# Kernel optimization log

Measured on AMD Instinct MI355X. Metric: run time of the kernel, lower is better.

Reference implementation:

```python
import jax, jax.numpy as jnp
import numpy as np

B, C, H, W, K = 64, 64, 32, 32, 512  # batch, embedding_dim, latent HxW, num_embeddings
COMMITMENT_COST = 0.25


def setup_inputs() -> dict:
    key = jax.random.key(0)
    k1, k2 = jax.random.split(key)
    inputs = jax.random.normal(k1, (B, C, H, W), dtype=jnp.float32)
    # nn.Embedding weight initialized uniform(-1/K, 1/K)
    weight = jax.random.uniform(k2, (K, C), minval=-1.0 / K, maxval=1.0 / K, dtype=jnp.float32)
    return {"inputs": inputs, "weight": weight}


def reference(inputs, weight):
    # NCHW -> NHWC
    x = jnp.transpose(inputs, (0, 2, 3, 1))  # [B,H,W,C]
    b, h, w, c = x.shape
    flat = x.reshape(-1, c)  # [N, C], N = B*H*W

    distances = (jnp.sum(flat * flat, axis=1, keepdims=True)
                 + jnp.sum(weight * weight, axis=1)[None, :]
                 - 2.0 * flat @ weight.T)

    idx = jnp.argmin(distances, axis=1)  # [N]
    encodings = jax.nn.one_hot(idx, weight.shape[0], dtype=flat.dtype)  # [N, K]

    # gather codebook vectors (same math as encodings @ weight)
    quantized = weight[idx].reshape(x.shape)  # [B,H,W,C]

    e_latent = jnp.mean((jax.lax.stop_gradient(quantized) - x) ** 2, axis=(1, 2, 3))
    q_latent = jnp.mean((quantized - jax.lax.stop_gradient(x)) ** 2, axis=(1, 2, 3))
    loss = q_latent + COMMITMENT_COST * e_latent  # [B]

    # straight-through estimator
    quantized_st = x + jax.lax.stop_gradient(quantized - x)

    avg_probs = jnp.mean(encodings, axis=0)  # [K]
    perplexity = jnp.exp(-jnp.sum(avg_probs * jnp.log(avg_probs + 1e-10)))

    q_out = jnp.transpose(quantized_st, (0, 3, 1, 2))  # back to NCHW
    enc_idx = idx.reshape(b, -1)  # [B, H*W]
    return (q_out, loss, perplexity, encodings, enc_idx, distances)
```

## Files before the change

kernel.cpp:

```cpp
#include <hip/hip_runtime.h>
#include <stdint.h>
#include <math.h>

#pragma clang fp contract(off)

#define B_   64
#define C_   64
#define HW_  1024
#define K_   512
#define N_   65536

#define OUT_Q    0ull
#define OUT_LOSS 4194304ull
#define OUT_PERP 4194368ull
#define OUT_ENC  4194369ull
#define OUT_IDX  37748801ull
#define OUT_DIST 37814337ull

#define WS_WT     0ull
#define WS_WNORM  131072ull
#define WS_HIST   133120ull
#define WS_SUMSQ  135168ull
#define WS_ZERO_BYTES (512*4 + 64*4)

__global__ __launch_bounds__(256) void vq_prep(const float* __restrict__ w,
                                               float* __restrict__ wt,
                                               float* __restrict__ wnorm) {
  const int t = threadIdx.x;
  const int g = blockIdx.x * 256 + t;
  const int c = g >> 9;
  const int k = g & 511;
  wt[g] = w[k * 64 + c];

  if (blockIdx.x < 16) {
    const int row = g >> 3;
    const int j = g & 7;
    float s = 0.f;
    for (int i = 0; i < 8; ++i) {
      float v = w[row * 64 + 8 * i + j];
      float sq = v * v;
      s = s + sq;
    }
    float o1 = __shfl_xor(s, 1); s = s + o1;
    float o2 = __shfl_xor(s, 2); s = s + o2;
    float o4 = __shfl_xor(s, 4); s = s + o4;
    if (j == 0) wnorm[row] = s;
  }
}

__global__ __launch_bounds__(256, 3) void vq_main(const float* __restrict__ x,
                                                  const float* __restrict__ wt,
                                                  const float* __restrict__ wnorm,
                                                  float* __restrict__ out,
                                                  int* __restrict__ hist,
                                                  float* __restrict__ sumsq) {
  __shared__ float x_s[64 * 32];
  __shared__ float w_s[16 * 512];
  __shared__ float wn_s[512];
  __shared__ float an_s[32];
  __shared__ int   kmin_s[32];
  __shared__ float red_s[4];

  const int t   = threadIdx.x;
  const int blk = blockIdx.x;
  const int n0  = blk * 32;
  const int b   = n0 >> 10;
  const int hw0 = n0 & 1023;
  const int wid = t >> 6;
  const int l   = t & 63;

  {
    const float* xb = x + (size_t)b * 65536 + hw0;
    const int c0 = t >> 3;
    const int m4 = (t & 7) * 4;
    for (int i = 0; i < 2; ++i) {
      int c = i * 32 + c0;
      float4 v = *(const float4*)(xb + (size_t)c * 1024 + m4);
      *(float4*)(&x_s[c * 32 + m4]) = v;
    }
  }
  wn_s[t] = wnorm[t];
  wn_s[t + 256] = wnorm[t + 256];
  __syncthreads();

  {
    const int r = t >> 3, j = t & 7;
    float s = 0.f;
    for (int i = 0; i < 8; ++i) {
      float v = x_s[(8 * i + j) * 32 + r];
      float sq = v * v;
      s = s + sq;
    }
    float o1 = __shfl_xor(s, 1); s = s + o1;
    float o2 = __shfl_xor(s, 2); s = s + o2;
    float o4 = __shfl_xor(s, 4); s = s + o4;
    if (j == 0) an_s[r] = s;
  }

  float wn[8];
  for (int j = 0; j < 8; ++j) wn[j] = wn_s[l + 64 * j];

  float acc[8][8];
  for (int i = 0; i < 8; ++i)
    for (int j = 0; j < 8; ++j) acc[i][j] = 0.f;

#pragma unroll 1
  for (int cc = 0; cc < 4; ++cc) {
    __syncthreads();
    for (int i = 0; i < 8; ++i) {
      int f4 = i * 256 + t;
      *(float4*)(&w_s[f4 * 4]) = *(const float4*)(wt + (size_t)cc * 8192 + f4 * 4);
    }
    __syncthreads();
#pragma unroll
    for (int cl = 0; cl < 16; ++cl) {
      const int c = cc * 16 + cl;
      float xv[8];
      *(float4*)(xv)     = *(const float4*)(&x_s[c * 32 + 8 * wid]);
      *(float4*)(xv + 4) = *(const float4*)(&x_s[c * 32 + 8 * wid + 4]);
      float wv[8];
      for (int j = 0; j < 8; ++j) wv[j] = w_s[cl * 512 + l + 64 * j];
      for (int i = 0; i < 8; ++i)
        for (int j = 0; j < 8; ++j)
          acc[i][j] = __builtin_fmaf(xv[i], wv[j], acc[i][j]);
    }
  }

  float* const dist_o = out + OUT_DIST;
  float* const enc_o  = out + OUT_ENC;
  const int m_base = 8 * wid;
  for (int i = 0; i < 8; ++i) {
    const int m = m_base + i;
    const size_t n = (size_t)(n0 + m);
    const float an = an_s[m];
    float D[8];
    for (int j = 0; j < 8; ++j) {
      float tt = an + wn[j];
      D[j] = __builtin_fmaf(-2.f, acc[i][j], tt);
    }
    float vb = D[0]; int kb = l;
    for (int j = 1; j < 8; ++j) {
      if (D[j] < vb) { vb = D[j]; kb = l + 64 * j; }
    }
    for (int d = 1; d < 64; d <<= 1) {
      float v2 = __shfl_xor(vb, d);
      int   k2 = __shfl_xor(kb, d);
      if (v2 < vb || (v2 == vb && k2 < kb)) { vb = v2; kb = k2; }
    }
    const size_t rb = n * 512 + l;
    for (int j = 0; j < 8; ++j) dist_o[rb + 64 * j] = D[j];
    for (int j = 0; j < 8; ++j) enc_o[rb + 64 * j] = (l + 64 * j == kb) ? 1.f : 0.f;
    if (l == i) {
      out[OUT_IDX + n] = (float)kb;
      atomicAdd(&hist[kb], 1);
      kmin_s[m] = kb;
    }
  }
  __syncthreads();

  float lsum = 0.f;
  float* const q_o = out + OUT_Q;
  for (int it = 0; it < 8; ++it) {
    const int idx8 = it * 256 + t;
    const int c = idx8 >> 5, m = idx8 & 31;
    const int kb = kmin_s[m];
    const float qv = wt[(size_t)c * 512 + kb];
    const float xv = x_s[c * 32 + m];
    const float d = qv - xv;
    lsum = __builtin_fmaf(d, d, lsum);
    q_o[(size_t)b * 65536 + (size_t)c * 1024 + (hw0 + m)] = qv;
  }
  for (int d = 1; d < 64; d <<= 1) lsum += __shfl_xor(lsum, d);
  if (l == 0) red_s[wid] = lsum;
  __syncthreads();
  if (t == 0) {
    float s = (red_s[0] + red_s[1]) + (red_s[2] + red_s[3]);
    atomicAdd(sumsq + b, s);
  }
}

__global__ __launch_bounds__(512) void vq_fin(const int* __restrict__ hist,
                                              const float* __restrict__ sumsq,
                                              float* __restrict__ out) {
  __shared__ double red[8];
  const int t = threadIdx.x;
  double p = (double)hist[t] * (1.0 / 65536.0);
  double term = p * log(p + 1e-10);
  for (int d = 1; d < 64; d <<= 1) term += __shfl_xor(term, d);
  if ((t & 63) == 0) red[t >> 6] = term;
  __syncthreads();
  if (t == 0) {
    double s = 0.0;
    for (int i = 0; i < 8; ++i) s += red[i];
    out[OUT_PERP] = (float)exp(-s);
  }
  if (t < 64) {
    float m = sumsq[t] * (1.0f / 65536.0f);
    out[OUT_LOSS + t] = m + 0.25f * m;
  }
}

extern "C" void kernel_launch(void* const* d_in, const int* in_sizes, int n_in,
                              void* d_out, int out_size, void* d_ws, size_t ws_size,
                              hipStream_t stream) {
  const float* x = (const float*)d_in[0];
  const float* w = (const float*)d_in[1];
  float* out = (float*)d_out;
  char* ws = (char*)d_ws;
  float* wt    = (float*)(ws + WS_WT);
  float* wnorm = (float*)(ws + WS_WNORM);
  int*   hist  = (int*)  (ws + WS_HIST);
  float* sumsq = (float*)(ws + WS_SUMSQ);

  (void)hipMemsetAsync(ws + WS_HIST, 0, WS_ZERO_BYTES, stream);
  vq_prep<<<128, 256, 0, stream>>>(w, wt, wnorm);
  vq_main<<<2048, 256, 0, stream>>>(x, wt, wnorm, out, hist, sumsq);
  vq_fin<<<1, 512, 0, stream>>>(hist, sumsq, out);
}
```

Before: 356.9 us.

## Relayout codebook for vector LDS reads, read x from global, move histogram to finalizer

Adds a second transposed codebook copy interleaved so each lane reads its 8 codewords as two float4 LDS loads instead of eight strided scalar loads. In the inner loop, x values now come straight from global/L1 through a wave-uniform pointer rather than from LDS. The global histogram atomics in the main kernel are dropped; the single-block finalizer rebuilds the histogram from the stored indices using privatized shared-memory counters. The memset is replaced by zeroing sumsq inside the prep kernel. The trade-off is that the finalizer now does serial work over all 65536 indices in one block, and the inner loop takes on global-load latency.

```diff
diff --git a/kernel.cpp b/kernel.cpp
--- a/kernel.cpp
+++ b/kernel.cpp
@@ -18,27 +18,32 @@
 #define OUT_DIST 37814337ull
 
 #define WS_WT     0ull
-#define WS_WNORM  131072ull
-#define WS_HIST   133120ull
-#define WS_SUMSQ  135168ull
-#define WS_ZERO_BYTES (512*4 + 64*4)
+#define WS_WT2    131072ull
+#define WS_WNORM  262144ull
+#define WS_SUMSQ  264192ull
 
 __global__ __launch_bounds__(256) void vq_prep(const float* __restrict__ w,
                                                float* __restrict__ wt,
-                                               float* __restrict__ wnorm) {
+                                               float* __restrict__ wt2,
+                                               float* __restrict__ wnorm,
+                                               float* __restrict__ sumsq) {
   const int t = threadIdx.x;
   const int g = blockIdx.x * 256 + t;
   const int c = g >> 9;
   const int k = g & 511;
-  wt[g] = w[k * 64 + c];
+  const float v = w[k * 64 + c];
+  wt[g] = v;
+  wt2[(c >> 4) * 8192 + (c & 15) * 512 + (k & 63) * 8 + (k >> 6)] = v;
+
+  if (blockIdx.x == 0 && t < 64) sumsq[t] = 0.f;
 
   if (blockIdx.x < 16) {
     const int row = g >> 3;
     const int j = g & 7;
     float s = 0.f;
     for (int i = 0; i < 8; ++i) {
-      float v = w[row * 64 + 8 * i + j];
-      float sq = v * v;
+      float vv = w[row * 64 + 8 * i + j];
+      float sq = vv * vv;
       s = s + sq;
     }
     float o1 = __shfl_xor(s, 1); s = s + o1;
@@ -50,9 +55,9 @@
 
 __global__ __launch_bounds__(256, 3) void vq_main(const float* __restrict__ x,
                                                   const float* __restrict__ wt,
+                                                  const float* __restrict__ wt2,
                                                   const float* __restrict__ wnorm,
                                                   float* __restrict__ out,
-                                                  int* __restrict__ hist,
                                                   float* __restrict__ sumsq) {
   __shared__ float x_s[64 * 32];
   __shared__ float w_s[16 * 512];
@@ -100,6 +105,9 @@
   float wn[8];
   for (int j = 0; j < 8; ++j) wn[j] = wn_s[l + 64 * j];
 
+  const int uwid = __builtin_amdgcn_readfirstlane(wid);
+  const float* xrow = x + (size_t)b * 65536 + (size_t)(hw0 + 8 * uwid);
+
   float acc[8][8];
   for (int i = 0; i < 8; ++i)
     for (int j = 0; j < 8; ++j) acc[i][j] = 0.f;
@@ -109,17 +117,18 @@
     __syncthreads();
     for (int i = 0; i < 8; ++i) {
       int f4 = i * 256 + t;
-      *(float4*)(&w_s[f4 * 4]) = *(const float4*)(wt + (size_t)cc * 8192 + f4 * 4);
+      *(float4*)(&w_s[f4 * 4]) = *(const float4*)(wt2 + (size_t)cc * 8192 + f4 * 4);
     }
     __syncthreads();
 #pragma unroll
     for (int cl = 0; cl < 16; ++cl) {
-      const int c = cc * 16 + cl;
+      const float* xp = xrow + (size_t)(cc * 16 + cl) * 1024;
       float xv[8];
-      *(float4*)(xv)     = *(const float4*)(&x_s[c * 32 + 8 * wid]);
-      *(float4*)(xv + 4) = *(const float4*)(&x_s[c * 32 + 8 * wid + 4]);
+      *(float4*)(xv)     = *(const float4*)(xp);
+      *(float4*)(xv + 4) = *(const float4*)(xp + 4);
       float wv[8];
-      for (int j = 0; j < 8; ++j) wv[j] = w_s[cl * 512 + l + 64 * j];
+      *(float4*)(wv)     = *(const float4*)(&w_s[cl * 512 + l * 8]);
+      *(float4*)(wv + 4) = *(const float4*)(&w_s[cl * 512 + l * 8 + 4]);
       for (int i = 0; i < 8; ++i)
         for (int j = 0; j < 8; ++j)
           acc[i][j] = __builtin_fmaf(xv[i], wv[j], acc[i][j]);
@@ -152,7 +161,6 @@
     for (int j = 0; j < 8; ++j) enc_o[rb + 64 * j] = (l + 64 * j == kb) ? 1.f : 0.f;
     if (l == i) {
       out[OUT_IDX + n] = (float)kb;
-      atomicAdd(&hist[kb], 1);
       kmin_s[m] = kb;
     }
   }
@@ -179,15 +187,27 @@
   }
 }
 
-__global__ __launch_bounds__(512) void vq_fin(const int* __restrict__ hist,
-                                              const float* __restrict__ sumsq,
-                                              float* __restrict__ out) {
+__global__ __launch_bounds__(1024) void vq_fin(float* __restrict__ out,
+                                               const float* __restrict__ sumsq) {
+  __shared__ int h4[4 * 512];
   __shared__ double red[8];
   const int t = threadIdx.x;
-  double p = (double)hist[t] * (1.0 / 65536.0);
-  double term = p * log(p + 1e-10);
-  for (int d = 1; d < 64; d <<= 1) term += __shfl_xor(term, d);
-  if ((t & 63) == 0) red[t >> 6] = term;
+  h4[t] = 0; h4[t + 1024] = 0;
+  __syncthreads();
+  const float* idxp = out + OUT_IDX;
+  int* const myh = &h4[(t & 3) * 512];
+  for (int i = t; i < 65536; i += 1024) {
+    int k = (int)idxp[i];
+    atomicAdd(&myh[k], 1);
+  }
+  __syncthreads();
+  if (t < 512) {
+    int cnt = h4[t] + h4[512 + t] + h4[1024 + t] + h4[1536 + t];
+    double p = (double)cnt * (1.0 / 65536.0);
+    double term = p * log(p + 1e-10);
+    for (int d = 1; d < 64; d <<= 1) term += __shfl_xor(term, d);
+    if ((t & 63) == 0) red[t >> 6] = term;
+  }
   __syncthreads();
   if (t == 0) {
     double s = 0.0;
@@ -208,12 +228,11 @@
   float* out = (float*)d_out;
   char* ws = (char*)d_ws;
   float* wt    = (float*)(ws + WS_WT);
+  float* wt2   = (float*)(ws + WS_WT2);
   float* wnorm = (float*)(ws + WS_WNORM);
-  int*   hist  = (int*)  (ws + WS_HIST);
   float* sumsq = (float*)(ws + WS_SUMSQ);
 
-  (void)hipMemsetAsync(ws + WS_HIST, 0, WS_ZERO_BYTES, stream);
-  vq_prep<<<128, 256, 0, stream>>>(w, wt, wnorm);
-  vq_main<<<2048, 256, 0, stream>>>(x, wt, wnorm, out, hist, sumsq);
-  vq_fin<<<1, 512, 0, stream>>>(hist, sumsq, out);
-}
+  vq_prep<<<128, 256, 0, stream>>>(w, wt, wt2, wnorm, sumsq);
+  vq_main<<<2048, 256, 0, stream>>>(x, wt, wt2, wnorm, out, sumsq);
+  vq_fin<<<1, 1024, 0, stream>>>(out, sumsq);
+}
```

New measurement: 365.3 us. +2.3%, slower.
